# Kernel tuning notes

Hardware: AMD Instinct MI355X
Metric: run time of the kernel (lower is better)

## Reference

```python
import jax, jax.numpy as jnp
import numpy as np

N_NODES = 50000
N_EDGES = 800000
FEATURES = 64
HIDDEN = 128
OUT_DIM = 64
CUTOFF = 10.0
STEP = 0.1
N_MU = 100  # len(arange(0, 10, 0.1))


def setup_inputs() -> dict:
    key = jax.random.key(0)
    k_h, k_src, k_dst, k_norm, k_w1, k_w2 = jax.random.split(key, 6)
    h = jax.random.normal(k_h, (N_NODES, FEATURES), dtype=jnp.float32)
    src = jax.random.randint(k_src, (N_EDGES,), 0, N_NODES, dtype=jnp.int64)
    dst = jax.random.randint(k_dst, (N_EDGES,), 0, N_NODES, dtype=jnp.int64)
    edge_norm = jax.random.uniform(k_norm, (N_EDGES,), dtype=jnp.float32) * CUTOFF
    mu = jnp.arange(0.0, CUTOFF, STEP, dtype=jnp.float32)  # [100], learned param
    in_dim = 2 * FEATURES + N_MU
    # xavier_normal with gain split across 2 linear layers: layer_gain = 1.0
    s1 = float(np.sqrt(2.0 / (in_dim + HIDDEN)))
    s2 = float(np.sqrt(2.0 / (HIDDEN + OUT_DIM)))
    W1 = jax.random.normal(k_w1, (HIDDEN, in_dim), dtype=jnp.float32) * s1
    W2 = jax.random.normal(k_w2, (OUT_DIM, HIDDEN), dtype=jnp.float32) * s2
    return {"h": h, "src": src, "dst": dst, "edge_norm": edge_norm,
            "mu": mu, "W1": W1, "W2": W2}


def reference(h, src, dst, edge_norm, mu, W1, W2):
    # Gaussian RBF expansion of edge distances: [E, n_mu]
    d_emb = jnp.exp((-1.0 / STEP) * (mu[None, :] - edge_norm[:, None]) ** 2)
    # gather endpoint features and concat: [E, 2*features + n_mu]
    x = jnp.concatenate((h[src], h[dst], d_emb), axis=-1)
    # MLP: Linear(no bias) -> SiLU -> Linear(no bias)
    hdn = jax.nn.silu(x @ W1.T)
    return hdn @ W2.T
```

## Files before the change

kernel.cpp:

```cpp
#include <hip/hip_runtime.h>
#include <hip/hip_bf16.h>


#define FEAT     64
#define NMU      100
#define K1_REAL  228
#define HID      128
#define ODIM     64
#define K2       128
#define WEDGES   32
#define BEDGES   128
#define LDH2     136
#define HN8      400000

typedef __bf16 bf16x8 __attribute__((ext_vector_type(8)));
typedef float  fx4    __attribute__((ext_vector_type(4)));

__global__ void pack_w(const float* __restrict__ W1, const float* __restrict__ W2,
                       __bf16* __restrict__ B1, __bf16* __restrict__ B2) {
    int i = blockIdx.x * 256 + threadIdx.x;
    if (i < 32768) {
        int j  = i & 7;
        int n  = (i >> 3) & 127;
        int qk = i >> 10;
        int k  = (qk >> 2) * 32 + (qk & 3) * 8 + j;
        float v = (k < K1_REAL) ? W1[n * K1_REAL + k] : 0.0f;
        B1[i] = (__bf16)v;
    } else {
        int t = i - 32768;
        int j  = t & 7;
        int n  = (t >> 3) & 63;
        int qk = t >> 9;
        int k  = (qk >> 2) * 32 + (qk & 3) * 8 + j;
        B2[t] = (__bf16)W2[n * K2 + k];
    }
}

__global__ void pack_h(const float* __restrict__ h, __bf16* __restrict__ hb) {
    int i = blockIdx.x * 256 + threadIdx.x;
    if (i >= HN8) return;
    const float4* p = (const float4*)h + (size_t)i * 2;
    float4 v0 = p[0];
    float4 v1 = p[1];
    bf16x8 b = { (__bf16)v0.x, (__bf16)v0.y, (__bf16)v0.z, (__bf16)v0.w,
                 (__bf16)v1.x, (__bf16)v1.y, (__bf16)v1.z, (__bf16)v1.w };
    ((bf16x8*)hb)[i] = b;
}

__device__ __forceinline__ bf16x8 hfrag_f32(const float* __restrict__ h, int node, int cb) {
    const float4* p = (const float4*)(h + (size_t)node * FEAT + cb);
    float4 v0 = p[0];
    float4 v1 = p[1];
    bf16x8 a = { (__bf16)v0.x, (__bf16)v0.y, (__bf16)v0.z, (__bf16)v0.w,
                 (__bf16)v1.x, (__bf16)v1.y, (__bf16)v1.z, (__bf16)v1.w };
    return a;
}

template<bool HB16>
__global__ __launch_bounds__(256, 4)
void edges_fused(const float* __restrict__ h,
                 const __bf16* __restrict__ hb,
                 const int*   __restrict__ src,
                 const int*   __restrict__ dst,
                 const float* __restrict__ enorm,
                 const float* __restrict__ mu,
                 const __bf16* __restrict__ B1,
                 const __bf16* __restrict__ B2,
                 float* __restrict__ out) {
    __shared__ __bf16 Hs[4 * WEDGES * LDH2];

    const int tid  = threadIdx.x;
    const int w    = tid >> 6;
    const int lane = tid & 63;
    const int ln   = lane & 15;
    const int q    = lane >> 4;
    const int g0   = blockIdx.x * BEDGES + w * WEDGES;

    int nsrc[2], ndst[2];
    float dval[2];
#pragma unroll
    for (int mt = 0; mt < 2; ++mt) {
        int e = g0 + mt * 16 + ln;
        nsrc[mt] = src[e];
        ndst[mt] = dst[e];
        dval[mt] = enorm[e];
    }

    fx4 acc1[2][8];
#pragma unroll
    for (int mt = 0; mt < 2; ++mt)
#pragma unroll
        for (int nt = 0; nt < 8; ++nt)
            acc1[mt][nt] = (fx4){0.f, 0.f, 0.f, 0.f};

    const bf16x8* pB1 = (const bf16x8*)B1;

#pragma unroll
    for (int kk = 0; kk < 4; ++kk) {
        const int cb = (kk & 1) * 32 + q * 8;
        bf16x8 a[2];
#pragma unroll
        for (int mt = 0; mt < 2; ++mt) {
            int node = (kk < 2) ? nsrc[mt] : ndst[mt];
            if constexpr (HB16)
                a[mt] = *(const bf16x8*)(hb + (size_t)node * FEAT + cb);
            else
                a[mt] = hfrag_f32(h, node, cb);
        }
#pragma unroll
        for (int nt = 0; nt < 8; ++nt) {
            bf16x8 b = pB1[(kk * 4 + q) * 128 + nt * 16 + ln];
            acc1[0][nt] = __builtin_amdgcn_mfma_f32_16x16x32_bf16(a[0], b, acc1[0][nt], 0, 0, 0);
            acc1[1][nt] = __builtin_amdgcn_mfma_f32_16x16x32_bf16(a[1], b, acc1[1][nt], 0, 0, 0);
        }
    }

#pragma unroll
    for (int kk = 4; kk < 7; ++kk) {
        const int c0 = (kk - 4) * 32 + q * 8;
        float4 m0 = *(const float4*)(mu + c0);
        float4 m1 = *(const float4*)(mu + c0 + 4);
        bf16x8 a[2];
#pragma unroll
        for (int mt = 0; mt < 2; ++mt) {
            float d = dval[mt];
            float t0 = m0.x - d, t1 = m0.y - d, t2 = m0.z - d, t3 = m0.w - d;
            float t4 = m1.x - d, t5 = m1.y - d, t6 = m1.z - d, t7 = m1.w - d;
            a[mt] = (bf16x8){ (__bf16)__expf(-10.f * t0 * t0), (__bf16)__expf(-10.f * t1 * t1),
                              (__bf16)__expf(-10.f * t2 * t2), (__bf16)__expf(-10.f * t3 * t3),
                              (__bf16)__expf(-10.f * t4 * t4), (__bf16)__expf(-10.f * t5 * t5),
                              (__bf16)__expf(-10.f * t6 * t6), (__bf16)__expf(-10.f * t7 * t7) };
        }
#pragma unroll
        for (int nt = 0; nt < 8; ++nt) {
            bf16x8 b = pB1[(kk * 4 + q) * 128 + nt * 16 + ln];
            acc1[0][nt] = __builtin_amdgcn_mfma_f32_16x16x32_bf16(a[0], b, acc1[0][nt], 0, 0, 0);
            acc1[1][nt] = __builtin_amdgcn_mfma_f32_16x16x32_bf16(a[1], b, acc1[1][nt], 0, 0, 0);
        }
    }

    {
        float4 m7 = *(const float4*)(mu + 96);
        const __bf16 zz = (__bf16)0.0f;
        const bool qz = (q == 0);
        bf16x8 a[2];
#pragma unroll
        for (int mt = 0; mt < 2; ++mt) {
            float d = dval[mt];
            float t0 = m7.x - d, t1 = m7.y - d, t2 = m7.z - d, t3 = m7.w - d;
            a[mt] = (bf16x8){ qz ? (__bf16)__expf(-10.f * t0 * t0) : zz,
                              qz ? (__bf16)__expf(-10.f * t1 * t1) : zz,
                              qz ? (__bf16)__expf(-10.f * t2 * t2) : zz,
                              qz ? (__bf16)__expf(-10.f * t3 * t3) : zz,
                              zz, zz, zz, zz };
        }
#pragma unroll
        for (int nt = 0; nt < 8; ++nt) {
            bf16x8 b = pB1[(7 * 4 + q) * 128 + nt * 16 + ln];
            acc1[0][nt] = __builtin_amdgcn_mfma_f32_16x16x32_bf16(a[0], b, acc1[0][nt], 0, 0, 0);
            acc1[1][nt] = __builtin_amdgcn_mfma_f32_16x16x32_bf16(a[1], b, acc1[1][nt], 0, 0, 0);
        }
    }

    __bf16* Hw = &Hs[w * WEDGES * LDH2];
#pragma unroll
    for (int mt = 0; mt < 2; ++mt)
#pragma unroll
        for (int nt = 0; nt < 8; ++nt)
#pragma unroll
            for (int r = 0; r < 4; ++r) {
                float z = acc1[mt][nt][r];
                float s = z * __builtin_amdgcn_rcpf(1.0f + __expf(-z));
                Hw[(mt * 16 + q * 4 + r) * LDH2 + nt * 16 + ln] = (__bf16)s;
            }

    fx4 acc2[2][4];
#pragma unroll
    for (int mt = 0; mt < 2; ++mt)
#pragma unroll
        for (int nt = 0; nt < 4; ++nt)
            acc2[mt][nt] = (fx4){0.f, 0.f, 0.f, 0.f};

    const bf16x8* pB2 = (const bf16x8*)B2;
#pragma unroll
    for (int kk = 0; kk < 4; ++kk) {
        bf16x8 a2[2];
#pragma unroll
        for (int mt = 0; mt < 2; ++mt)
            a2[mt] = *(const bf16x8*)&Hw[(mt * 16 + ln) * LDH2 + kk * 32 + q * 8];
#pragma unroll
        for (int nt = 0; nt < 4; ++nt) {
            bf16x8 b2 = pB2[(kk * 4 + q) * 64 + nt * 16 + ln];
            acc2[0][nt] = __builtin_amdgcn_mfma_f32_16x16x32_bf16(a2[0], b2, acc2[0][nt], 0, 0, 0);
            acc2[1][nt] = __builtin_amdgcn_mfma_f32_16x16x32_bf16(a2[1], b2, acc2[1][nt], 0, 0, 0);
        }
    }

#pragma unroll
    for (int mt = 0; mt < 2; ++mt)
#pragma unroll
        for (int nt = 0; nt < 4; ++nt)
#pragma unroll
            for (int r = 0; r < 4; ++r)
                out[(size_t)(g0 + mt * 16 + q * 4 + r) * ODIM + nt * 16 + ln] = acc2[mt][nt][r];
}

extern "C" void kernel_launch(void* const* d_in, const int* in_sizes, int n_in,
                              void* d_out, int out_size, void* d_ws, size_t ws_size,
                              hipStream_t stream) {
    const float* h   = (const float*)d_in[0];
    const int*   src = (const int*)d_in[1];
    const int*   dst = (const int*)d_in[2];
    const float* en  = (const float*)d_in[3];
    const float* mu  = (const float*)d_in[4];
    const float* W1  = (const float*)d_in[5];
    const float* W2  = (const float*)d_in[6];

    __bf16* B1 = (__bf16*)d_ws;
    __bf16* B2 = (__bf16*)((char*)d_ws + 65536);
    __bf16* HB = (__bf16*)((char*)d_ws + 81920);

    const size_t ws_needed = 81920 + (size_t)HN8 * 8 * sizeof(__bf16);
    const bool   use_hb    = ws_size >= ws_needed;

    pack_w<<<160, 256, 0, stream>>>(W1, W2, B1, B2);

    const int E = in_sizes[1];
    const int nblocks = E / BEDGES;

    if (use_hb) {
        pack_h<<<(HN8 + 255) / 256, 256, 0, stream>>>(h, HB);
        edges_fused<true><<<nblocks, 256, 0, stream>>>(h, HB, src, dst, en, mu, B1, B2, (float*)d_out);
    } else {
        edges_fused<false><<<nblocks, 256, 0, stream>>>(h, nullptr, src, dst, en, mu, B1, B2, (float*)d_out);
    }
}
```

Baseline: 357.3 us.

## Stage packed weights in LDS and hoist neighbor gathers before MFMA loop

Each block now copies the packed bf16 W1 and W2 into shared memory once and reads MFMA B fragments from LDS instead of global or L2. Block size doubles to 8 waves (256 edges), so each weight copy serves twice as many edges. All neighbor feature gathers are issued up front so their latency overlaps with the weight copy. This costs about 150 KB of LDS per block and adds a block-wide barrier, which cuts occupancy to roughly one block per CU and may expose gather latency.

```diff
diff --git a/kernel.cpp b/kernel.cpp
--- a/kernel.cpp
+++ b/kernel.cpp
@@ -9,7 +9,8 @@
 #define ODIM     64
 #define K2       128
 #define WEDGES   32
-#define BEDGES   128
+#define NWAVES   8
+#define BEDGES   (WEDGES * NWAVES)
 #define LDH2     136
 #define HN8      400000
 
@@ -57,7 +58,7 @@
 }
 
 template<bool HB16>
-__global__ __launch_bounds__(256, 4)
+__global__ __launch_bounds__(512, 2)
 void edges_fused(const float* __restrict__ h,
                  const __bf16* __restrict__ hb,
                  const int*   __restrict__ src,
@@ -67,7 +68,9 @@
                  const __bf16* __restrict__ B1,
                  const __bf16* __restrict__ B2,
                  float* __restrict__ out) {
-    __shared__ __bf16 Hs[4 * WEDGES * LDH2];
+    __shared__ __bf16 B1s[32768];
+    __shared__ __bf16 B2s[8192];
+    __shared__ __bf16 Hs[NWAVES * WEDGES * LDH2];
 
     const int tid  = threadIdx.x;
     const int w    = tid >> 6;
@@ -86,32 +89,52 @@
         dval[mt] = enorm[e];
     }
 
-    fx4 acc1[2][8];
-#pragma unroll
-    for (int mt = 0; mt < 2; ++mt)
-#pragma unroll
-        for (int nt = 0; nt < 8; ++nt)
-            acc1[mt][nt] = (fx4){0.f, 0.f, 0.f, 0.f};
-
-    const bf16x8* pB1 = (const bf16x8*)B1;
-
+    bf16x8 ag[4][2];
 #pragma unroll
     for (int kk = 0; kk < 4; ++kk) {
         const int cb = (kk & 1) * 32 + q * 8;
-        bf16x8 a[2];
 #pragma unroll
         for (int mt = 0; mt < 2; ++mt) {
             int node = (kk < 2) ? nsrc[mt] : ndst[mt];
             if constexpr (HB16)
-                a[mt] = *(const bf16x8*)(hb + (size_t)node * FEAT + cb);
+                ag[kk][mt] = *(const bf16x8*)(hb + (size_t)node * FEAT + cb);
             else
-                a[mt] = hfrag_f32(h, node, cb);
-        }
+                ag[kk][mt] = hfrag_f32(h, node, cb);
+        }
+    }
+
+    {
+        const bf16x8* gB1 = (const bf16x8*)B1;
+        const bf16x8* gB2 = (const bf16x8*)B2;
+        bf16x8* sB1 = (bf16x8*)B1s;
+        bf16x8* sB2 = (bf16x8*)B2s;
+#pragma unroll
+        for (int it = 0; it < 8; ++it) {
+            int g = it * 512 + tid;
+            sB1[g] = gB1[g];
+        }
+#pragma unroll
+        for (int it = 0; it < 2; ++it) {
+            int g = it * 512 + tid;
+            sB2[g] = gB2[g];
+        }
+    }
+    __syncthreads();
+
+    fx4 acc1[2][8];
+#pragma unroll
+    for (int mt = 0; mt < 2; ++mt)
+#pragma unroll
+        for (int nt = 0; nt < 8; ++nt)
+            acc1[mt][nt] = (fx4){0.f, 0.f, 0.f, 0.f};
+
+#pragma unroll
+    for (int kk = 0; kk < 4; ++kk) {
 #pragma unroll
         for (int nt = 0; nt < 8; ++nt) {
-            bf16x8 b = pB1[(kk * 4 + q) * 128 + nt * 16 + ln];
-            acc1[0][nt] = __builtin_amdgcn_mfma_f32_16x16x32_bf16(a[0], b, acc1[0][nt], 0, 0, 0);
-            acc1[1][nt] = __builtin_amdgcn_mfma_f32_16x16x32_bf16(a[1], b, acc1[1][nt], 0, 0, 0);
+            bf16x8 b = *(const bf16x8*)&B1s[(((kk * 4 + q) * 128) + nt * 16 + ln) * 8];
+            acc1[0][nt] = __builtin_amdgcn_mfma_f32_16x16x32_bf16(ag[kk][0], b, acc1[0][nt], 0, 0, 0);
+            acc1[1][nt] = __builtin_amdgcn_mfma_f32_16x16x32_bf16(ag[kk][1], b, acc1[1][nt], 0, 0, 0);
         }
     }
 
@@ -133,7 +156,7 @@
         }
 #pragma unroll
         for (int nt = 0; nt < 8; ++nt) {
-            bf16x8 b = pB1[(kk * 4 + q) * 128 + nt * 16 + ln];
+            bf16x8 b = *(const bf16x8*)&B1s[(((kk * 4 + q) * 128) + nt * 16 + ln) * 8];
             acc1[0][nt] = __builtin_amdgcn_mfma_f32_16x16x32_bf16(a[0], b, acc1[0][nt], 0, 0, 0);
             acc1[1][nt] = __builtin_amdgcn_mfma_f32_16x16x32_bf16(a[1], b, acc1[1][nt], 0, 0, 0);
         }
@@ -156,7 +179,7 @@
         }
 #pragma unroll
         for (int nt = 0; nt < 8; ++nt) {
-            bf16x8 b = pB1[(7 * 4 + q) * 128 + nt * 16 + ln];
+            bf16x8 b = *(const bf16x8*)&B1s[(((7 * 4 + q) * 128) + nt * 16 + ln) * 8];
             acc1[0][nt] = __builtin_amdgcn_mfma_f32_16x16x32_bf16(a[0], b, acc1[0][nt], 0, 0, 0);
             acc1[1][nt] = __builtin_amdgcn_mfma_f32_16x16x32_bf16(a[1], b, acc1[1][nt], 0, 0, 0);
         }
@@ -181,7 +204,6 @@
         for (int nt = 0; nt < 4; ++nt)
             acc2[mt][nt] = (fx4){0.f, 0.f, 0.f, 0.f};
 
-    const bf16x8* pB2 = (const bf16x8*)B2;
 #pragma unroll
     for (int kk = 0; kk < 4; ++kk) {
         bf16x8 a2[2];
@@ -190,7 +212,7 @@
             a2[mt] = *(const bf16x8*)&Hw[(mt * 16 + ln) * LDH2 + kk * 32 + q * 8];
 #pragma unroll
         for (int nt = 0; nt < 4; ++nt) {
-            bf16x8 b2 = pB2[(kk * 4 + q) * 64 + nt * 16 + ln];
+            bf16x8 b2 = *(const bf16x8*)&B2s[(((kk * 4 + q) * 64) + nt * 16 + ln) * 8];
             acc2[0][nt] = __builtin_amdgcn_mfma_f32_16x16x32_bf16(a2[0], b2, acc2[0][nt], 0, 0, 0);
             acc2[1][nt] = __builtin_amdgcn_mfma_f32_16x16x32_bf16(a2[1], b2, acc2[1][nt], 0, 0, 0);
         }
@@ -230,8 +252,8 @@
 
     if (use_hb) {
         pack_h<<<(HN8 + 255) / 256, 256, 0, stream>>>(h, HB);
-        edges_fused<true><<<nblocks, 256, 0, stream>>>(h, HB, src, dst, en, mu, B1, B2, (float*)d_out);
+        edges_fused<true><<<nblocks, 512, 0, stream>>>(h, HB, src, dst, en, mu, B1, B2, (float*)d_out);
     } else {
-        edges_fused<false><<<nblocks, 256, 0, stream>>>(h, nullptr, src, dst, en, mu, B1, B2, (float*)d_out);
-    }
-}
+        edges_fused<false><<<nblocks, 512, 0, stream>>>(h, nullptr, src, dst, en, mu, B1, B2, (float*)d_out);
+    }
+}
```

Result: faster. 328.2 us (-8.2%).
